# Kernel tuning notes

Measured on AMD Instinct MI355X. Metric: run time of the kernel, lower is better.

Reference implementation:

```python
import jax, jax.numpy as jnp
import numpy as np

BATCH, NUM_POINTS, DIM, NUM_PROJS = 32, 4096, 3, 256


def _sobol_2d(n):
    """Unscrambled 2D Sobol sequence (Joe-Kuo direction numbers), first point = 0,
    matching torch.quasirandom.SobolEngine(dimension=2, scramble=False).draw(n)."""
    bits = 32
    V = np.zeros((2, bits), dtype=np.uint64)
    for j in range(bits):
        V[0, j] = np.uint64(1) << np.uint64(bits - 1 - j)  # van der Corput
    m = [1]
    for i in range(1, bits):
        m.append((2 * m[i - 1]) ^ m[i - 1])  # s=1, a=0 recurrence -> 1,3,5,15,17,...
    for j in range(bits):
        V[1, j] = np.uint64(m[j]) << np.uint64(bits - 1 - j)
    x = np.zeros(2, dtype=np.uint64)
    pts = np.zeros((n, 2), dtype=np.float64)
    for i in range(1, n):
        c, v = 0, i - 1
        while v & 1:
            v >>= 1
            c += 1
        x ^= V[:, c]
        pts[i] = x / float(2 ** bits)
    return pts


def setup_inputs() -> dict:
    key = jax.random.key(0)
    kx, ky, kr = jax.random.split(key, 3)
    x = jax.random.normal(kx, (BATCH, NUM_POINTS, DIM), dtype=jnp.float32)
    y = jax.random.normal(ky, (BATCH, NUM_POINTS, DIM), dtype=jnp.float32)

    # Sobol points -> uniform directions on S^2 (as in the torch module)
    net = _sobol_2d(NUM_PROJS)
    alpha, tau = net[:, 0], net[:, 1]
    r = 2.0 * np.sqrt(np.clip(tau - tau ** 2, 0.0, None))
    theta = np.stack([r * np.cos(2 * np.pi * alpha),
                      r * np.sin(2 * np.pi * alpha),
                      1.0 - 2.0 * tau], axis=1).astype(np.float32)  # [P,3]

    # Per-sample random rotation: Q of QR(randn(3,3)), batched
    g = np.asarray(jax.random.normal(kr, (BATCH, DIM, DIM), dtype=jnp.float32))
    rotations = np.linalg.qr(g.astype(np.float64))[0].astype(np.float32)  # [B,3,3]

    return {"x": x, "y": y, "theta": jnp.asarray(theta), "rotations": jnp.asarray(rotations)}


def reference(x, y, theta, rotations):
    # rotated projections: [B, P, 3]
    proj = jnp.einsum('pd,bde->bpe', theta, rotations)
    # project point clouds: [B, P, N]
    xp = jnp.einsum('bnd,bpd->bpn', x, proj)
    yp = jnp.einsum('bnd,bpd->bpn', y, proj)
    # sorted 1D Wasserstein-2 per projection
    d = jnp.sort(xp, axis=-1) - jnp.sort(yp, axis=-1)
    per_proj = jnp.sum(d * d, axis=-1)              # [B, P]  (|.|^2, degree=2)
    dist = jnp.sqrt(jnp.mean(per_proj, axis=1))     # [B]
    return jnp.mean(dist)
```

## Files before the change

kernel.cpp:

```cpp
#include <hip/hip_runtime.h>
#include <math.h>

#define NPTS 4096
#define BLK 128
#define V 64
#define NPROJ 256
#define NBATCH 32


__device__ __forceinline__ void cmpex_asc(float& a, float& b) {
    const float lo = fminf(a, b), hi = fmaxf(a, b);
    a = lo; b = hi;
}

template<int JB, int JL>
__device__ __forceinline__ void stages(float* v) {
#pragma unroll
    for (int r = 0; r < V; ++r)
        if ((r & JB) == 0) cmpex_asc(v[r], v[r | JB]);
    if constexpr (JB > JL) stages<(JB >> 1), JL>(v);
}

template<int MASK>
__device__ __forceinline__ void rev_inreg(float* v) {
    constexpr int S = (MASK + 1) >> 1;
#pragma unroll
    for (int r = 0; r < V; ++r) {
        if ((r & S) == 0) {
            const float a = v[r], b = v[r ^ MASK];
            v[r] = fminf(a, b);
            v[r ^ MASK] = fmaxf(a, b);
        }
    }
}

template<int XM>
__device__ __forceinline__ void rev_shfl(float* v, bool hi) {
#pragma unroll
    for (int r = 0; r < 32; ++r) {
        const float pa = __shfl_xor(v[63 - r], XM, 64);
        const float pb = __shfl_xor(v[r], XM, 64);
        v[r]      = hi ? fmaxf(v[r], pa)      : fminf(v[r], pa);
        v[63 - r] = hi ? fmaxf(v[63 - r], pb) : fminf(v[63 - r], pb);
    }
}
template<int XM>
__device__ __forceinline__ void stage_shfl(float* v, bool hi) {
#pragma unroll
    for (int r = 0; r < V; ++r) {
        const float q = __shfl_xor(v[r], XM, 64);
        v[r] = hi ? fmaxf(v[r], q) : fminf(v[r], q);
    }
}

__device__ __forceinline__ void write_AB(float* s, const float* v, int sAB, int t15) {
    float4* s4 = (float4*)s;
#pragma unroll
    for (int c = 0; c < 16; ++c)
        s4[sAB | (c << 4) | (t15 ^ c)] =
            make_float4(v[4*c], v[4*c+1], v[4*c+2], v[4*c+3]);
}
__device__ __forceinline__ void write_own(float* s, const float* v, int t, int t15) {
    float4* s4 = (float4*)s;
#pragma unroll
    for (int c = 0; c < 16; ++c)
        s4[(t << 4) | (c ^ t15)] =
            make_float4(v[4*c], v[4*c+1], v[4*c+2], v[4*c+3]);
}
__device__ __forceinline__ void read_own(const float* s, float* v, int t, int t15) {
    const float4* s4 = (const float4*)s;
#pragma unroll
    for (int c = 0; c < 16; ++c) {
        const float4 f = s4[(t << 4) | (c ^ t15)];
        v[4*c] = f.x; v[4*c+1] = f.y; v[4*c+2] = f.z; v[4*c+3] = f.w;
    }
}
template<int PM, int CM, int KB>
__device__ __forceinline__ void read_rev_B(const float* s, float* v, int t, int t15, bool thi) {
    const float4* s4 = (const float4*)s;
    const int pt = t ^ PM, pt15 = t15 ^ (PM & 15);
#pragma unroll
    for (int c = 0; c < 16; ++c) {
        const float4 o = s4[(t << 4) | (c ^ t15)];
        const float4 q = s4[(pt << 4) | ((c ^ CM) ^ pt15)];
        const bool mx = KB ? ((c & KB) != 0) : thi;
        v[4*c+0] = mx ? fmaxf(o.x, q.w) : fminf(o.x, q.w);
        v[4*c+1] = mx ? fmaxf(o.y, q.z) : fminf(o.y, q.z);
        v[4*c+2] = mx ? fmaxf(o.z, q.y) : fminf(o.z, q.y);
        v[4*c+3] = mx ? fmaxf(o.w, q.x) : fminf(o.w, q.x);
    }
}
__device__ __forceinline__ void write_AC(float* s, const float* v, int t15, int qAC) {
    float4* s4 = (float4*)s;
#pragma unroll
    for (int c = 0; c < 16; ++c)
        s4[(t15 << 6) | ((c >> 2) << 4) | (qAC ^ (c & 3))] =
            make_float4(v[4*c], v[4*c+1], v[4*c+2], v[4*c+3]);
}
__device__ __forceinline__ void read_rev_C(const float* s, float* v, int t, int th) {
    const float4* s4 = (const float4*)s;
    const int pt = t ^ 63, pth = th ^ 15;
#pragma unroll
    for (int c = 0; c < 16; ++c) {
        const float4 o = s4[(t << 4) | (c ^ th)];
        const float4 q = s4[(pt << 4) | ((c ^ 15) ^ pth)];
        const bool mx = (c & 8) != 0;
        v[4*c+0] = mx ? fmaxf(o.x, q.w) : fminf(o.x, q.w);
        v[4*c+1] = mx ? fmaxf(o.y, q.z) : fminf(o.y, q.z);
        v[4*c+2] = mx ? fmaxf(o.z, q.y) : fminf(o.z, q.y);
        v[4*c+3] = mx ? fmaxf(o.w, q.x) : fminf(o.w, q.x);
    }
}
__device__ __forceinline__ void write_CB(float* s, const float* v, int sCB, int qCB) {
    float4* s4 = (float4*)s;
#pragma unroll
    for (int c = 0; c < 16; ++c)
        s4[((c >> 2) << 8) | sCB | ((c & 3) << 4) | (qCB ^ (c & 3))] =
            make_float4(v[4*c], v[4*c+1], v[4*c+2], v[4*c+3]);
}

__device__ __forceinline__ void sort4096(float* v, float* buf, int t) {
    const int t15 = t & 15;
    const int sAB = (t >> 4) << 8;
    const int qAC = ((t >> 4) << 2) ^ t15;
    const int th  = (t >> 2) & 15;
    const int sCB = (t & 3) << 6;
    const int qCB = (t >> 2) ^ ((t & 3) << 2);
    const bool hi1  = (t & 1) != 0;
    const bool hi2  = (t & 2) != 0;
    const bool hi16 = (t & 16) != 0;

    rev_inreg<1>(v);
    rev_inreg<3>(v);  stages<1, 1>(v);
    rev_inreg<7>(v);  stages<2, 1>(v);
    rev_inreg<15>(v); stages<4, 1>(v);
    rev_inreg<31>(v); stages<8, 1>(v);
    rev_inreg<63>(v); stages<16, 1>(v);

    rev_shfl<1>(v, hi1);
    stages<32, 1>(v);

    rev_shfl<3>(v, hi2);
    stage_shfl<2>(v, hi2);
    stage_shfl<1>(v, hi1);
    stages<32, 1>(v);

    write_AB(buf, v, sAB, t15);
    read_rev_B<15, 7, 4>(buf, v, t, t15, false);
    stages<8, 4>(v);
    write_AB(buf, v, sAB, t15);
    read_own(buf, v, t, t15);
    stages<32, 1>(v);

    write_AB(buf, v, sAB, t15);
    read_rev_B<15, 15, 8>(buf, v, t, t15, false);
    stages<16, 4>(v);
    write_AB(buf, v, sAB, t15);
    read_own(buf, v, t, t15);
    stages<32, 1>(v);

    write_AB(buf, v, sAB, t15);
    read_rev_B<31, 15, 0>(buf, v, t, t15, hi16);
    stages<32, 4>(v);
    write_AB(buf, v, sAB, t15);
    read_own(buf, v, t, t15);
    stages<32, 1>(v);

    write_AC(buf, v, t15, qAC);
    read_rev_C(buf, v, t, th);
    stages<16, 16>(v);
    write_CB(buf, v, sCB, qCB);
    read_own(buf, v, t, t15);
    stages<32, 4>(v);
    write_AB(buf, v, sAB, t15);
    read_own(buf, v, t, t15);
    stages<32, 1>(v);
}

__device__ __forceinline__ void load_project(const float* base, float* v,
                                             float p0, float p1, float p2) {
    const float4* b4 = (const float4*)base;
#pragma unroll
    for (int g = 0; g < 16; ++g) {
        float4 a = b4[g * 3 + 0], c = b4[g * 3 + 1], d = b4[g * 3 + 2];
        v[4*g+0] = a.x * p0 + a.y * p1 + a.z * p2;
        v[4*g+1] = a.w * p0 + c.x * p1 + c.y * p2;
        v[4*g+2] = c.z * p0 + c.w * p1 + d.x * p2;
        v[4*g+3] = d.y * p0 + d.z * p1 + d.w * p2;
    }
}

__global__ __launch_bounds__(BLK, 2) void swd_kernel(
    const float* __restrict__ x, const float* __restrict__ y,
    const float* __restrict__ theta, const float* __restrict__ rot,
    float* __restrict__ per_batch) {
    __shared__ float buf2[2][NPTS];

    const int t = threadIdx.x & 63;
    const int wave = threadIdx.x >> 6;
    const int p = blockIdx.x;
    const int b = blockIdx.y;

    const float t0 = theta[p * 3 + 0], t1 = theta[p * 3 + 1], t2 = theta[p * 3 + 2];
    const float* R = rot + b * 9;
    const float p0 = t0 * R[0] + t1 * R[3] + t2 * R[6];
    const float p1 = t0 * R[1] + t1 * R[4] + t2 * R[7];
    const float p2 = t0 * R[2] + t1 * R[5] + t2 * R[8];

    float* buf = buf2[wave];
    const float* src = wave ? y : x;

    float v[V];
    load_project(src + (size_t)b * NPTS * 3 + (size_t)t * V * 3, v, p0, p1, p2);
    sort4096(v, buf, t);

    const int t15 = t & 15;
    if (wave == 1) write_own(buf2[1], v, t, t15);
    __syncthreads();

    if (wave == 0) {
        float w[V];
        read_own(buf2[1], w, t, t15);
        float s = 0.0f;
#pragma unroll
        for (int r = 0; r < V; ++r) {
            const float d = v[r] - w[r];
            s += d * d;
        }
        for (int off = 32; off > 0; off >>= 1) s += __shfl_down(s, off, 64);
        if (t == 0) atomicAdd(&per_batch[b], s);
    }
}

__global__ void finalize_kernel(const float* __restrict__ per_batch, float* __restrict__ out) {
    const int t = threadIdx.x;
    float v = (t < NBATCH) ? sqrtf(per_batch[t] * (1.0f / (float)NPROJ)) : 0.0f;
    for (int off = 32; off > 0; off >>= 1) v += __shfl_down(v, off, 64);
    if (t == 0) out[0] = v * (1.0f / (float)NBATCH);
}

extern "C" void kernel_launch(void* const* d_in, const int* in_sizes, int n_in,
                              void* d_out, int out_size, void* d_ws, size_t ws_size,
                              hipStream_t stream) {
    const float* x = (const float*)d_in[0];
    const float* y = (const float*)d_in[1];
    const float* theta = (const float*)d_in[2];
    const float* rot = (const float*)d_in[3];
    float* per_batch = (float*)d_ws;
    float* out = (float*)d_out;

    hipMemsetAsync(per_batch, 0, NBATCH * sizeof(float), stream);

    dim3 grid(NPROJ, NBATCH);
    swd_kernel<<<grid, BLK, 0, stream>>>(x, y, theta, rot, per_batch);

    finalize_kernel<<<1, 64, 0, stream>>>(per_batch, out);
}
```

Baseline: 369.6 us.

## Share one LDS buffer between waves with ping-pong staggered exchange phases

Result: slower. 1.000 ms (+170.6%).

```diff
diff --git a/kernel.cpp b/kernel.cpp
--- a/kernel.cpp
+++ b/kernel.cpp
@@ -119,7 +119,41 @@
             make_float4(v[4*c], v[4*c+1], v[4*c+2], v[4*c+3]);
 }
 
-__device__ __forceinline__ void sort4096(float* v, float* buf, int t) {
+__device__ __forceinline__ void load_project(const float* base, float* v,
+                                             float p0, float p1, float p2) {
+    const float4* b4 = (const float4*)base;
+#pragma unroll
+    for (int g = 0; g < 16; ++g) {
+        float4 a = b4[g * 3 + 0], c = b4[g * 3 + 1], d = b4[g * 3 + 2];
+        v[4*g+0] = a.x * p0 + a.y * p1 + a.z * p2;
+        v[4*g+1] = a.w * p0 + c.x * p1 + c.y * p2;
+        v[4*g+2] = c.z * p0 + c.w * p1 + d.x * p2;
+        v[4*g+3] = d.y * p0 + d.z * p1 + d.w * p2;
+    }
+}
+
+__global__ __launch_bounds__(BLK, 5) void swd_kernel(
+    const float* __restrict__ x, const float* __restrict__ y,
+    const float* __restrict__ theta, const float* __restrict__ rot,
+    float* __restrict__ per_batch) {
+    __shared__ float buf[NPTS];
+
+    const int t = threadIdx.x & 63;
+    const int wave = threadIdx.x >> 6;
+    const int p = blockIdx.x;
+    const int b = blockIdx.y;
+
+    const float t0 = theta[p * 3 + 0], t1 = theta[p * 3 + 1], t2 = theta[p * 3 + 2];
+    const float* R = rot + b * 9;
+    const float p0 = t0 * R[0] + t1 * R[3] + t2 * R[6];
+    const float p1 = t0 * R[1] + t1 * R[4] + t2 * R[7];
+    const float p2 = t0 * R[2] + t1 * R[5] + t2 * R[8];
+
+    const float* src = wave ? y : x;
+
+    float v[V];
+    load_project(src + (size_t)b * NPTS * 3 + (size_t)t * V * 3, v, p0, p1, p2);
+
     const int t15 = t & 15;
     const int sAB = (t >> 4) << 8;
     const int qAC = ((t >> 4) << 2) ^ t15;
@@ -136,91 +170,73 @@
     rev_inreg<15>(v); stages<4, 1>(v);
     rev_inreg<31>(v); stages<8, 1>(v);
     rev_inreg<63>(v); stages<16, 1>(v);
-
     rev_shfl<1>(v, hi1);
     stages<32, 1>(v);
-
     rev_shfl<3>(v, hi2);
     stage_shfl<2>(v, hi2);
     stage_shfl<1>(v, hi1);
     stages<32, 1>(v);
 
-    write_AB(buf, v, sAB, t15);
-    read_rev_B<15, 7, 4>(buf, v, t, t15, false);
-    stages<8, 4>(v);
-    write_AB(buf, v, sAB, t15);
-    read_own(buf, v, t, t15);
-    stages<32, 1>(v);
-
-    write_AB(buf, v, sAB, t15);
-    read_rev_B<15, 15, 8>(buf, v, t, t15, false);
-    stages<16, 4>(v);
-    write_AB(buf, v, sAB, t15);
-    read_own(buf, v, t, t15);
-    stages<32, 1>(v);
-
-    write_AB(buf, v, sAB, t15);
-    read_rev_B<31, 15, 0>(buf, v, t, t15, hi16);
-    stages<32, 4>(v);
-    write_AB(buf, v, sAB, t15);
-    read_own(buf, v, t, t15);
-    stages<32, 1>(v);
-
-    write_AC(buf, v, t15, qAC);
-    read_rev_C(buf, v, t, th);
-    stages<16, 16>(v);
-    write_CB(buf, v, sCB, qCB);
-    read_own(buf, v, t, t15);
-    stages<32, 4>(v);
-    write_AB(buf, v, sAB, t15);
-    read_own(buf, v, t, t15);
-    stages<32, 1>(v);
-}
-
-__device__ __forceinline__ void load_project(const float* base, float* v,
-                                             float p0, float p1, float p2) {
-    const float4* b4 = (const float4*)base;
-#pragma unroll
-    for (int g = 0; g < 16; ++g) {
-        float4 a = b4[g * 3 + 0], c = b4[g * 3 + 1], d = b4[g * 3 + 2];
-        v[4*g+0] = a.x * p0 + a.y * p1 + a.z * p2;
-        v[4*g+1] = a.w * p0 + c.x * p1 + c.y * p2;
-        v[4*g+2] = c.z * p0 + c.w * p1 + d.x * p2;
-        v[4*g+3] = d.y * p0 + d.z * p1 + d.w * p2;
-    }
-}
-
-__global__ __launch_bounds__(BLK, 2) void swd_kernel(
-    const float* __restrict__ x, const float* __restrict__ y,
-    const float* __restrict__ theta, const float* __restrict__ rot,
-    float* __restrict__ per_batch) {
-    __shared__ float buf2[2][NPTS];
-
-    const int t = threadIdx.x & 63;
-    const int wave = threadIdx.x >> 6;
-    const int p = blockIdx.x;
-    const int b = blockIdx.y;
-
-    const float t0 = theta[p * 3 + 0], t1 = theta[p * 3 + 1], t2 = theta[p * 3 + 2];
-    const float* R = rot + b * 9;
-    const float p0 = t0 * R[0] + t1 * R[3] + t2 * R[6];
-    const float p1 = t0 * R[1] + t1 * R[4] + t2 * R[7];
-    const float p2 = t0 * R[2] + t1 * R[5] + t2 * R[8];
-
-    float* buf = buf2[wave];
-    const float* src = wave ? y : x;
-
-    float v[V];
-    load_project(src + (size_t)b * NPTS * 3 + (size_t)t * V * 3, v, p0, p1, p2);
-    sort4096(v, buf, t);
-
-    const int t15 = t & 15;
-    if (wave == 1) write_own(buf2[1], v, t, t15);
+
+    if (wave == 0) { write_AB(buf, v, sAB, t15); read_rev_B<15, 7, 4>(buf, v, t, t15, false); }
+    __syncthreads();
+    if (wave == 0) { stages<8, 4>(v); }
+    else           { write_AB(buf, v, sAB, t15); read_rev_B<15, 7, 4>(buf, v, t, t15, false); }
+    __syncthreads();
+    if (wave == 0) { write_AB(buf, v, sAB, t15); read_own(buf, v, t, t15); }
+    else           { stages<8, 4>(v); }
+    __syncthreads();
+    if (wave == 0) { stages<32, 1>(v); }
+    else           { write_AB(buf, v, sAB, t15); read_own(buf, v, t, t15); }
+    __syncthreads();
+    if (wave == 0) { write_AB(buf, v, sAB, t15); read_rev_B<15, 15, 8>(buf, v, t, t15, false); }
+    else           { stages<32, 1>(v); }
+    __syncthreads();
+    if (wave == 0) { stages<16, 4>(v); }
+    else           { write_AB(buf, v, sAB, t15); read_rev_B<15, 15, 8>(buf, v, t, t15, false); }
+    __syncthreads();
+    if (wave == 0) { write_AB(buf, v, sAB, t15); read_own(buf, v, t, t15); }
+    else           { stages<16, 4>(v); }
+    __syncthreads();
+    if (wave == 0) { stages<32, 1>(v); }
+    else           { write_AB(buf, v, sAB, t15); read_own(buf, v, t, t15); }
+    __syncthreads();
+    if (wave == 0) { write_AB(buf, v, sAB, t15); read_rev_B<31, 15, 0>(buf, v, t, t15, hi16); }
+    else           { stages<32, 1>(v); }
+    __syncthreads();
+    if (wave == 0) { stages<32, 4>(v); }
+    else           { write_AB(buf, v, sAB, t15); read_rev_B<31, 15, 0>(buf, v, t, t15, hi16); }
+    __syncthreads();
+    if (wave == 0) { write_AB(buf, v, sAB, t15); read_own(buf, v, t, t15); }
+    else           { stages<32, 4>(v); }
+    __syncthreads();
+    if (wave == 0) { stages<32, 1>(v); }
+    else           { write_AB(buf, v, sAB, t15); read_own(buf, v, t, t15); }
+    __syncthreads();
+    if (wave == 0) { write_AC(buf, v, t15, qAC); read_rev_C(buf, v, t, th); }
+    else           { stages<32, 1>(v); }
+    __syncthreads();
+    if (wave == 0) { stages<16, 16>(v); }
+    else           { write_AC(buf, v, t15, qAC); read_rev_C(buf, v, t, th); }
+    __syncthreads();
+    if (wave == 0) { write_CB(buf, v, sCB, qCB); read_own(buf, v, t, t15); }
+    else           { stages<16, 16>(v); }
+    __syncthreads();
+    if (wave == 0) { stages<32, 4>(v); }
+    else           { write_CB(buf, v, sCB, qCB); read_own(buf, v, t, t15); }
+    __syncthreads();
+    if (wave == 0) { write_AB(buf, v, sAB, t15); read_own(buf, v, t, t15); }
+    else           { stages<32, 4>(v); }
+    __syncthreads();
+    if (wave == 0) { stages<32, 1>(v); }
+    else           { write_AB(buf, v, sAB, t15); read_own(buf, v, t, t15); }
+    __syncthreads();
+    if (wave == 1) { stages<32, 1>(v); write_own(buf, v, t, t15); }
     __syncthreads();
 
     if (wave == 0) {
         float w[V];
-        read_own(buf2[1], w, t, t15);
+        read_own(buf, w, t, t15);
         float s = 0.0f;
 #pragma unroll
         for (int r = 0; r < V; ++r) {
```

## Replace LDS-based cross-lane merge stages with DPP/shuffle bitonic exchanges

Applied to the files above, without the earlier changes.

Result: no change. 365.1 us (-1.2%).

```diff
diff --git a/kernel.cpp b/kernel.cpp
--- a/kernel.cpp
+++ b/kernel.cpp
@@ -53,13 +53,6 @@
     }
 }
 
-__device__ __forceinline__ void write_AB(float* s, const float* v, int sAB, int t15) {
-    float4* s4 = (float4*)s;
-#pragma unroll
-    for (int c = 0; c < 16; ++c)
-        s4[sAB | (c << 4) | (t15 ^ c)] =
-            make_float4(v[4*c], v[4*c+1], v[4*c+2], v[4*c+3]);
-}
 __device__ __forceinline__ void write_own(float* s, const float* v, int t, int t15) {
     float4* s4 = (float4*)s;
 #pragma unroll
@@ -75,60 +68,27 @@
         v[4*c] = f.x; v[4*c+1] = f.y; v[4*c+2] = f.z; v[4*c+3] = f.w;
     }
 }
-template<int PM, int CM, int KB>
-__device__ __forceinline__ void read_rev_B(const float* s, float* v, int t, int t15, bool thi) {
-    const float4* s4 = (const float4*)s;
-    const int pt = t ^ PM, pt15 = t15 ^ (PM & 15);
+
+__device__ __forceinline__ void load_project(const float* base, float* v,
+                                             float p0, float p1, float p2) {
+    const float4* b4 = (const float4*)base;
 #pragma unroll
-    for (int c = 0; c < 16; ++c) {
-        const float4 o = s4[(t << 4) | (c ^ t15)];
-        const float4 q = s4[(pt << 4) | ((c ^ CM) ^ pt15)];
-        const bool mx = KB ? ((c & KB) != 0) : thi;
-        v[4*c+0] = mx ? fmaxf(o.x, q.w) : fminf(o.x, q.w);
-        v[4*c+1] = mx ? fmaxf(o.y, q.z) : fminf(o.y, q.z);
-        v[4*c+2] = mx ? fmaxf(o.z, q.y) : fminf(o.z, q.y);
-        v[4*c+3] = mx ? fmaxf(o.w, q.x) : fminf(o.w, q.x);
+    for (int g = 0; g < 16; ++g) {
+        float4 a = b4[g * 3 + 0], c = b4[g * 3 + 1], d = b4[g * 3 + 2];
+        v[4*g+0] = a.x * p0 + a.y * p1 + a.z * p2;
+        v[4*g+1] = a.w * p0 + c.x * p1 + c.y * p2;
+        v[4*g+2] = c.z * p0 + c.w * p1 + d.x * p2;
+        v[4*g+3] = d.y * p0 + d.z * p1 + d.w * p2;
     }
 }
-__device__ __forceinline__ void write_AC(float* s, const float* v, int t15, int qAC) {
-    float4* s4 = (float4*)s;
-#pragma unroll
-    for (int c = 0; c < 16; ++c)
-        s4[(t15 << 6) | ((c >> 2) << 4) | (qAC ^ (c & 3))] =
-            make_float4(v[4*c], v[4*c+1], v[4*c+2], v[4*c+3]);
-}
-__device__ __forceinline__ void read_rev_C(const float* s, float* v, int t, int th) {
-    const float4* s4 = (const float4*)s;
-    const int pt = t ^ 63, pth = th ^ 15;
-#pragma unroll
-    for (int c = 0; c < 16; ++c) {
-        const float4 o = s4[(t << 4) | (c ^ th)];
-        const float4 q = s4[(pt << 4) | ((c ^ 15) ^ pth)];
-        const bool mx = (c & 8) != 0;
-        v[4*c+0] = mx ? fmaxf(o.x, q.w) : fminf(o.x, q.w);
-        v[4*c+1] = mx ? fmaxf(o.y, q.z) : fminf(o.y, q.z);
-        v[4*c+2] = mx ? fmaxf(o.z, q.y) : fminf(o.z, q.y);
-        v[4*c+3] = mx ? fmaxf(o.w, q.x) : fminf(o.w, q.x);
-    }
-}
-__device__ __forceinline__ void write_CB(float* s, const float* v, int sCB, int qCB) {
-    float4* s4 = (float4*)s;
-#pragma unroll
-    for (int c = 0; c < 16; ++c)
-        s4[((c >> 2) << 8) | sCB | ((c & 3) << 4) | (qCB ^ (c & 3))] =
-            make_float4(v[4*c], v[4*c+1], v[4*c+2], v[4*c+3]);
-}
 
-__device__ __forceinline__ void sort4096(float* v, float* buf, int t) {
-    const int t15 = t & 15;
-    const int sAB = (t >> 4) << 8;
-    const int qAC = ((t >> 4) << 2) ^ t15;
-    const int th  = (t >> 2) & 15;
-    const int sCB = (t & 3) << 6;
-    const int qCB = (t >> 2) ^ ((t & 3) << 2);
+__device__ __forceinline__ void sort4096(float* v, int t) {
     const bool hi1  = (t & 1) != 0;
     const bool hi2  = (t & 2) != 0;
+    const bool hi4  = (t & 4) != 0;
+    const bool hi8  = (t & 8) != 0;
     const bool hi16 = (t & 16) != 0;
+    const bool hi32 = (t & 32) != 0;
 
     rev_inreg<1>(v);
     rev_inreg<3>(v);  stages<1, 1>(v);
@@ -145,56 +105,38 @@
     stage_shfl<1>(v, hi1);
     stages<32, 1>(v);
 
-    write_AB(buf, v, sAB, t15);
-    read_rev_B<15, 7, 4>(buf, v, t, t15, false);
-    stages<8, 4>(v);
-    write_AB(buf, v, sAB, t15);
-    read_own(buf, v, t, t15);
+    rev_shfl<7>(v, hi4);
+    stage_shfl<2>(v, hi2);
+    stage_shfl<1>(v, hi1);
     stages<32, 1>(v);
 
-    write_AB(buf, v, sAB, t15);
-    read_rev_B<15, 15, 8>(buf, v, t, t15, false);
-    stages<16, 4>(v);
-    write_AB(buf, v, sAB, t15);
-    read_own(buf, v, t, t15);
+    rev_shfl<15>(v, hi8);
+    stage_shfl<4>(v, hi4);
+    stage_shfl<2>(v, hi2);
+    stage_shfl<1>(v, hi1);
     stages<32, 1>(v);
 
-    write_AB(buf, v, sAB, t15);
-    read_rev_B<31, 15, 0>(buf, v, t, t15, hi16);
-    stages<32, 4>(v);
-    write_AB(buf, v, sAB, t15);
-    read_own(buf, v, t, t15);
+    rev_shfl<31>(v, hi16);
+    stage_shfl<8>(v, hi8);
+    stage_shfl<4>(v, hi4);
+    stage_shfl<2>(v, hi2);
+    stage_shfl<1>(v, hi1);
     stages<32, 1>(v);
 
-    write_AC(buf, v, t15, qAC);
-    read_rev_C(buf, v, t, th);
-    stages<16, 16>(v);
-    write_CB(buf, v, sCB, qCB);
-    read_own(buf, v, t, t15);
-    stages<32, 4>(v);
-    write_AB(buf, v, sAB, t15);
-    read_own(buf, v, t, t15);
+    rev_shfl<63>(v, hi32);
+    stage_shfl<16>(v, hi16);
+    stage_shfl<8>(v, hi8);
+    stage_shfl<4>(v, hi4);
+    stage_shfl<2>(v, hi2);
+    stage_shfl<1>(v, hi1);
     stages<32, 1>(v);
-}
-
-__device__ __forceinline__ void load_project(const float* base, float* v,
-                                             float p0, float p1, float p2) {
-    const float4* b4 = (const float4*)base;
-#pragma unroll
-    for (int g = 0; g < 16; ++g) {
-        float4 a = b4[g * 3 + 0], c = b4[g * 3 + 1], d = b4[g * 3 + 2];
-        v[4*g+0] = a.x * p0 + a.y * p1 + a.z * p2;
-        v[4*g+1] = a.w * p0 + c.x * p1 + c.y * p2;
-        v[4*g+2] = c.z * p0 + c.w * p1 + d.x * p2;
-        v[4*g+3] = d.y * p0 + d.z * p1 + d.w * p2;
-    }
 }
 
 __global__ __launch_bounds__(BLK, 2) void swd_kernel(
     const float* __restrict__ x, const float* __restrict__ y,
     const float* __restrict__ theta, const float* __restrict__ rot,
     float* __restrict__ per_batch) {
-    __shared__ float buf2[2][NPTS];
+    __shared__ float buf[NPTS];
 
     const int t = threadIdx.x & 63;
     const int wave = threadIdx.x >> 6;
@@ -207,20 +149,19 @@
     const float p1 = t0 * R[1] + t1 * R[4] + t2 * R[7];
     const float p2 = t0 * R[2] + t1 * R[5] + t2 * R[8];
 
-    float* buf = buf2[wave];
     const float* src = wave ? y : x;
 
     float v[V];
     load_project(src + (size_t)b * NPTS * 3 + (size_t)t * V * 3, v, p0, p1, p2);
-    sort4096(v, buf, t);
+    sort4096(v, t);
 
     const int t15 = t & 15;
-    if (wave == 1) write_own(buf2[1], v, t, t15);
+    if (wave == 1) write_own(buf, v, t, t15);
     __syncthreads();
 
     if (wave == 0) {
         float w[V];
-        read_own(buf2[1], w, t, t15);
+        read_own(buf, w, t, t15);
         float s = 0.0f;
 #pragma unroll
         for (int r = 0; r < V; ++r) {
```
